# Optimization experiments

Measured on AMD Instinct MI355X. Metric: run time of the kernel, lower is better.

## Reference

```python
import jax, jax.numpy as jnp
import numpy as np

# Problem dimensions (match init_kwargs / input_specs)
B, NT = 4, 256          # shots, timesteps
NZ, NX = 384, 384       # domain
NREC = 128              # receivers
DT, DH = 0.001, 10.0    # time step [s], grid spacing [m]


def setup_inputs() -> dict:
    key = jax.random.key(0)
    k1, k2, k3, k4, k5, k6 = jax.random.split(key, 6)
    # source wavelets, one per shot: [B, NT]
    x = jax.random.normal(k1, (B, NT), dtype=jnp.float32)
    # velocity model 1500..3500 m/s: [NZ, NX]
    vp = 1500.0 + 2000.0 * jax.random.uniform(k2, (NZ, NX), dtype=jnp.float32)
    # per-shot source locations (kept away from the boundary)
    src_y = jax.random.randint(k3, (B,), 20, NZ - 20, dtype=jnp.int32)
    src_x = jax.random.randint(k4, (B,), 20, NX - 20, dtype=jnp.int32)
    # shared receiver array
    rec_y = jax.random.randint(k5, (NREC,), 20, NZ - 20, dtype=jnp.int32)
    rec_x = jax.random.randint(k6, (NREC,), 20, NX - 20, dtype=jnp.int32)
    return {"x": x, "vp": vp, "src_y": src_y, "src_x": src_x,
            "rec_y": rec_y, "rec_x": rec_x}


def _laplacian(u, inv_dh2):
    # 5-point stencil with zero (Dirichlet) boundaries; u: [B, NZ, NX]
    l = (u[:, 2:, 1:-1] + u[:, :-2, 1:-1]
         + u[:, 1:-1, 2:] + u[:, 1:-1, :-2]
         - 4.0 * u[:, 1:-1, 1:-1]) * inv_dh2
    return jnp.pad(l, ((0, 0), (1, 1), (1, 1)))


def reference(x, vp, src_y, src_x, rec_y, rec_x):
    """Second-order acoustic wave time-stepping with scatter source injection
    and receiver gather, as in WaveRNN.forward. Returns [NT, B, NREC] traces."""
    c2dt2 = (vp * DT) ** 2            # [NZ, NX], broadcast over shots
    inv_dh2 = jnp.float32(1.0 / (DH * DH))
    bidx = jnp.arange(B)

    def step(carry, xt):
        h1, h2 = carry                # current / previous wavefields [B,NZ,NX]
        hn = 2.0 * h1 - h2 + c2dt2 * _laplacian(h1, inv_dh2)
        hn = hn.at[bidx, src_y, src_x].add(xt)   # source injection (smask scatter)
        rec = hn[:, rec_y, rec_x]                 # receiver gather [B, NREC]
        return (hn, h1), rec

    h0 = jnp.zeros((B, NZ, NX), dtype=x.dtype)
    (_, _), y = jax.lax.scan(jax.checkpoint(step), (h0, h0), x.T)  # scan over time
    return y  # [NT, B, NREC]
```

## Files before the change

kernel.cpp:

```cpp
#include <hip/hip_runtime.h>

#define BB 4
#define NT 256
#define NZ 384
#define NX 384
#define NREC 128
#define NZX (NZ*NX)
#define BNZX (BB*NZX)
#define DT 0.001f
#define INV_DH2 0.01f

#define TILE 48
#define HALO 8
#define REGN 64
#define NBLK 256
#define NTHR 512
#define FSTRIDE 16

__global__ void wave_init(unsigned* flags) {
    int i = blockIdx.x * blockDim.x + threadIdx.x;
    if (i < NBLK * FSTRIDE) flags[i] = 0u;
}

__device__ inline float dpp_shl1(float v) {
    return __int_as_float(__builtin_amdgcn_update_dpp(
        0, __float_as_int(v), 0x130 , 0xf, 0xf, true));
}
__device__ inline float dpp_shr1(float v) {
    return __int_as_float(__builtin_amdgcn_update_dpp(
        0, __float_as_int(v), 0x138 , 0xf, 0xf, true));
}

__device__ inline void grid_sync(unsigned* flags, unsigned gen, int nbId) {
    __syncthreads();
    if (threadIdx.x < 64) {
        if (threadIdx.x == 0)
            __hip_atomic_store(&flags[blockIdx.x * FSTRIDE], gen,
                               __ATOMIC_RELAXED, __HIP_MEMORY_SCOPE_AGENT);
        for (;;) {
            unsigned f = __hip_atomic_load(&flags[nbId * FSTRIDE],
                             __ATOMIC_RELAXED, __HIP_MEMORY_SCOPE_AGENT);
            if (__all(f >= gen)) break;
            __builtin_amdgcn_s_sleep(1);
        }
    }
    __syncthreads();
}

__global__ __launch_bounds__(NTHR)
void wave_tiled(float* __restrict__ ws, const float* __restrict__ vp,
                const float* __restrict__ x,
                const int* __restrict__ src_y, const int* __restrict__ src_x,
                const int* __restrict__ rec_y, const int* __restrict__ rec_x,
                float* __restrict__ y) {
    __shared__ float bnd[2][16][REGN];
    __shared__ float recBuf[NREC][8];
    __shared__ float xs[NT];
    __shared__ int recLoc[NREC], recOut[NREC];
    __shared__ int recCnt;

    unsigned* flags = (unsigned*)(ws + 4*BNZX);

    const int tid = threadIdx.x;
    const int col = tid & 63;
    const int w   = tid >> 6;
    const int r0  = w << 3;
    const int blk = blockIdx.x;
    const int b  = blk >> 6;
    const int tz = (blk >> 3) & 7;
    const int tx = blk & 7;
    const int oz = tz*TILE - HALO, ox = tx*TILE - HALO;
    const int gx = ox + col;
    const int sy = src_y[b], sx = src_x[b];

    if (tid == 0) recCnt = 0;
    for (int k = tid; k < 16*REGN; k += NTHR) ((float*)bnd[0])[k] = 0.f;
    for (int k = tid; k < NT; k += NTHR) xs[k] = x[b*NT + k];
    __syncthreads();
    for (int r = tid; r < NREC; r += NTHR) {
        int ry = rec_y[r], rx = rec_x[r];
        if (ry/TILE == tz && rx/TILE == tx) {
            int p = atomicAdd(&recCnt, 1);
            recLoc[p] = ((ry - oz) << 6) | (rx - ox);
            recOut[p] = b*NREC + r;
        }
    }
    __syncthreads();

    int myN = 0, myM[4], myP[4];
    bool ovf = false;
    for (int p = 0; p < recCnt; ++p) {
        int rl = recLoc[p];
        if ((rl & 63) == col) {
            int rm = (rl >> 6) - r0;
            if ((unsigned)rm < 8u) {
                if (myN < 4) { myM[myN] = rm; myP[myN] = p; ++myN; }
                else ovf = true;
            }
        }
    }

    int nbId = blk;
    if (tid < 8) {
        int d = tid + (tid >= 4);
        int nz2 = tz + d/3 - 1, nx2 = tx + d%3 - 1;
        if ((unsigned)nz2 < 8u && (unsigned)nx2 < 8u)
            nbId = (b << 6) | (nz2 << 3) | nx2;
    }

    float cur[8], prv[8], c2i[8];
    #pragma unroll
    for (int m = 0; m < 8; ++m) {
        cur[m] = 0.f; prv[m] = 0.f;
        const int gz = oz + r0 + m;
        const bool inner = (gz > 0 && gz < NZ-1 && gx > 0 && gx < NX-1);
        const float v = inner ? vp[gz*NX + gx] * DT : 0.f;
        c2i[m] = v * v * INV_DH2;
    }
    const bool srcCol = (gx == sx);
    const int  srcM   = sy - oz - r0;
    const int  iuUp   = (2*w-1 < 0) ? 0 : 2*w-1;
    const int  iuDn   = (2*w+2 > 15) ? 15 : 2*w+2;
    __syncthreads();

    #pragma unroll 1
    for (int t = 0; t < NT; ++t) {
        const int pr = t & 1, pw = pr ^ 1;
        const float upB = bnd[pr][iuUp][col];
        const float dnB = bnd[pr][iuDn][col];

        float hn[8];
        #pragma unroll
        for (int m = 0; m < 8; ++m) {
            const float ce = cur[m];
            const float up = (m == 0) ? upB : cur[m-1];
            const float dn = (m == 7) ? dnB : cur[m+1];
            const float lf = dpp_shl1(ce);
            const float rt = dpp_shr1(ce);
            const float s  = (up + dn) + (lf + rt);
            hn[m] = fmaf(2.f, ce, -prv[m]) + c2i[m] * fmaf(-4.f, ce, s);
        }
        #pragma unroll
        for (int m = 0; m < 8; ++m) { prv[m] = cur[m]; cur[m] = hn[m]; }

        if (srcCol && (unsigned)srcM < 8u) {
            const float xv = xs[t];
            #pragma unroll
            for (int m = 0; m < 8; ++m) if (m == srcM) cur[m] += xv;
        }
        {
            const int s2 = t & 7;
            if (ovf) {
                for (int p = 0; p < recCnt; ++p) {
                    int rl = recLoc[p];
                    if ((rl & 63) == col) {
                        int rm = (rl >> 6) - r0;
                        if ((unsigned)rm < 8u) {
                            float v = cur[0];
                            #pragma unroll
                            for (int m = 1; m < 8; ++m) if (rm == m) v = cur[m];
                            recBuf[p][s2] = v;
                        }
                    }
                }
            } else {
                #pragma unroll
                for (int k = 0; k < 4; ++k) {
                    if (k < myN) {
                        float v = cur[0];
                        #pragma unroll
                        for (int m = 1; m < 8; ++m) if (myM[k] == m) v = cur[m];
                        recBuf[myP[k]][s2] = v;
                    }
                }
            }
        }
        bnd[pw][2*w  ][col] = cur[0];
        bnd[pw][2*w+1][col] = cur[7];

        if ((t & 7) == 7) {
            const int o = t >> 3;
            __syncthreads();
            for (int k = tid; k < recCnt*8; k += NTHR) {
                int p = k >> 3, s2 = k & 7;
                y[(size_t)((o<<3)+s2)*(BB*NREC) + recOut[p]] = recBuf[p][s2];
            }
            if (t < NT-1) {
                float* Gc = ws + (size_t)(o & 1) * 2*BNZX;
                float* Gp = Gc + BNZX;
                const bool colF = (col >= HALO   && col < REGN-HALO);
                const bool colM = (col >= 2*HALO && col < REGN-2*HALO);
                #pragma unroll
                for (int m = 0; m < 8; ++m) {
                    const int i = r0 + m;
                    const bool rowF = (i >= HALO   && i < REGN-HALO);
                    const bool rowM = (i >= 2*HALO && i < REGN-2*HALO);
                    if (colF && rowF && !(colM && rowM)) {
                        const size_t g = (size_t)b*NZX + (size_t)(oz+i)*NX + gx;
                        __hip_atomic_store(&Gc[g], cur[m],
                                           __ATOMIC_RELAXED, __HIP_MEMORY_SCOPE_AGENT);
                        __hip_atomic_store(&Gp[g], prv[m],
                                           __ATOMIC_RELAXED, __HIP_MEMORY_SCOPE_AGENT);
                    }
                }
                grid_sync(flags, (unsigned)(o + 1), nbId);
                const bool colH = (col < HALO || col >= REGN-HALO);
                const bool gxIn = (gx >= 0 && gx < NX);
                #pragma unroll
                for (int m = 0; m < 8; ++m) {
                    const int i = r0 + m;
                    if (colH || i < HALO || i >= REGN-HALO) {
                        const int gz = oz + i;
                        if (gxIn && gz >= 0 && gz < NZ) {
                            const size_t g = (size_t)b*NZX + (size_t)gz*NX + gx;
                            cur[m] = __hip_atomic_load(&Gc[g],
                                         __ATOMIC_RELAXED, __HIP_MEMORY_SCOPE_AGENT);
                            prv[m] = __hip_atomic_load(&Gp[g],
                                         __ATOMIC_RELAXED, __HIP_MEMORY_SCOPE_AGENT);
                        } else { cur[m] = 0.f; prv[m] = 0.f; }
                    }
                }
                bnd[pw][2*w  ][col] = cur[0];
                bnd[pw][2*w+1][col] = cur[7];
            }
        }
        __syncthreads();
    }
}

extern "C" void kernel_launch(void* const* d_in, const int* in_sizes, int n_in,
                              void* d_out, int out_size, void* d_ws, size_t ws_size,
                              hipStream_t stream) {
    const float* x     = (const float*)d_in[0];
    const float* vp    = (const float*)d_in[1];
    const int*   src_y = (const int*)d_in[2];
    const int*   src_x = (const int*)d_in[3];
    const int*   rec_y = (const int*)d_in[4];
    const int*   rec_x = (const int*)d_in[5];
    float* y  = (float*)d_out;
    float* ws = (float*)d_ws;

    wave_init<<<(NBLK*FSTRIDE + 255)/256, 256, 0, stream>>>((unsigned*)(ws + 4*BNZX));
    wave_tiled<<<NBLK, NTHR, 0, stream>>>(ws, vp, x, src_y, src_x, rec_y, rec_x, y);
}
```

Before: 275.4 us.

## Pack halo exchange into 64-bit stores and overlap receiver writes with grid sync

The separate cur/prv halo arrays are interleaved into one 64-bit word per cell, halving the number of atomic stores and loads during the periodic halo exchange. The receiver trace flush now runs on non-polling warps while the first wavefront spins on neighbor flags, and the s_sleep in the spin loop is removed. Halo loads use clamped addresses so all eight loads can be issued before they are consumed. In exchange, the tight spin loop without sleep may add memory traffic, and the layout needs a wider workspace stride.

```diff
diff --git a/kernel.cpp b/kernel.cpp
--- a/kernel.cpp
+++ b/kernel.cpp
@@ -31,20 +31,13 @@
         0, __float_as_int(v), 0x138 , 0xf, 0xf, true));
 }
 
-__device__ inline void grid_sync(unsigned* flags, unsigned gen, int nbId) {
-    __syncthreads();
-    if (threadIdx.x < 64) {
-        if (threadIdx.x == 0)
-            __hip_atomic_store(&flags[blockIdx.x * FSTRIDE], gen,
-                               __ATOMIC_RELAXED, __HIP_MEMORY_SCOPE_AGENT);
-        for (;;) {
-            unsigned f = __hip_atomic_load(&flags[nbId * FSTRIDE],
-                             __ATOMIC_RELAXED, __HIP_MEMORY_SCOPE_AGENT);
-            if (__all(f >= gen)) break;
-            __builtin_amdgcn_s_sleep(1);
-        }
-    }
-    __syncthreads();
+__device__ inline void stg2(unsigned long long* p, float a, float b) {
+    unsigned long long v = (unsigned long long)__float_as_uint(a)
+                         | ((unsigned long long)__float_as_uint(b) << 32);
+    __hip_atomic_store(p, v, __ATOMIC_RELAXED, __HIP_MEMORY_SCOPE_AGENT);
+}
+__device__ inline unsigned long long ldg2(const unsigned long long* p) {
+    return __hip_atomic_load(p, __ATOMIC_RELAXED, __HIP_MEMORY_SCOPE_AGENT);
 }
 
 __global__ __launch_bounds__(NTHR)
@@ -60,6 +53,8 @@
     __shared__ int recCnt;
 
     unsigned* flags = (unsigned*)(ws + 4*BNZX);
+    unsigned long long* F[2] = { (unsigned long long*)ws,
+                                 (unsigned long long*)ws + BNZX };
 
     const int tid = threadIdx.x;
     const int col = tid & 63;
@@ -121,6 +116,8 @@
     const int  srcM   = sy - oz - r0;
     const int  iuUp   = (2*w-1 < 0) ? 0 : 2*w-1;
     const int  iuDn   = (2*w+2 > 15) ? 15 : 2*w+2;
+    const bool gxIn = (gx >= 0 && gx < NX);
+    const int  gxc  = min(max(gx, 0), NX-1);
     __syncthreads();
 
     #pragma unroll 1
@@ -180,14 +177,8 @@
 
         if ((t & 7) == 7) {
             const int o = t >> 3;
-            __syncthreads();
-            for (int k = tid; k < recCnt*8; k += NTHR) {
-                int p = k >> 3, s2 = k & 7;
-                y[(size_t)((o<<3)+s2)*(BB*NREC) + recOut[p]] = recBuf[p][s2];
-            }
             if (t < NT-1) {
-                float* Gc = ws + (size_t)(o & 1) * 2*BNZX;
-                float* Gp = Gc + BNZX;
+                unsigned long long* Fw = F[o & 1];
                 const bool colF = (col >= HALO   && col < REGN-HALO);
                 const bool colM = (col >= 2*HALO && col < REGN-2*HALO);
                 #pragma unroll
@@ -195,33 +186,55 @@
                     const int i = r0 + m;
                     const bool rowF = (i >= HALO   && i < REGN-HALO);
                     const bool rowM = (i >= 2*HALO && i < REGN-2*HALO);
-                    if (colF && rowF && !(colM && rowM)) {
-                        const size_t g = (size_t)b*NZX + (size_t)(oz+i)*NX + gx;
-                        __hip_atomic_store(&Gc[g], cur[m],
+                    if (colF && rowF && !(colM && rowM))
+                        stg2(&Fw[(size_t)b*NZX + (size_t)(oz+i)*NX + gx],
+                             cur[m], prv[m]);
+                }
+                __syncthreads();
+                if (tid < 64) {
+                    if (tid == 0)
+                        __hip_atomic_store(&flags[blk * FSTRIDE], (unsigned)(o+1),
                                            __ATOMIC_RELAXED, __HIP_MEMORY_SCOPE_AGENT);
-                        __hip_atomic_store(&Gp[g], prv[m],
-                                           __ATOMIC_RELAXED, __HIP_MEMORY_SCOPE_AGENT);
-                    }
-                }
-                grid_sync(flags, (unsigned)(o + 1), nbId);
+                    for (;;) {
+                        unsigned f = __hip_atomic_load(&flags[nbId * FSTRIDE],
+                                         __ATOMIC_RELAXED, __HIP_MEMORY_SCOPE_AGENT);
+                        if (__all(f >= (unsigned)(o+1))) break;
+                    }
+                } else {
+                    for (int k = tid - 64; k < recCnt*8; k += NTHR - 64) {
+                        int p = k >> 3, s2 = k & 7;
+                        y[(size_t)((o<<3)+s2)*(BB*NREC) + recOut[p]] = recBuf[p][s2];
+                    }
+                }
+                __syncthreads();
                 const bool colH = (col < HALO || col >= REGN-HALO);
-                const bool gxIn = (gx >= 0 && gx < NX);
+                unsigned long long tmp[8];
+                bool ringm[8], valm[8];
                 #pragma unroll
                 for (int m = 0; m < 8; ++m) {
                     const int i = r0 + m;
-                    if (colH || i < HALO || i >= REGN-HALO) {
-                        const int gz = oz + i;
-                        if (gxIn && gz >= 0 && gz < NZ) {
-                            const size_t g = (size_t)b*NZX + (size_t)gz*NX + gx;
-                            cur[m] = __hip_atomic_load(&Gc[g],
-                                         __ATOMIC_RELAXED, __HIP_MEMORY_SCOPE_AGENT);
-                            prv[m] = __hip_atomic_load(&Gp[g],
-                                         __ATOMIC_RELAXED, __HIP_MEMORY_SCOPE_AGENT);
-                        } else { cur[m] = 0.f; prv[m] = 0.f; }
+                    const int gz = oz + i;
+                    ringm[m] = colH || i < HALO || i >= REGN-HALO;
+                    valm[m]  = gxIn && gz >= 0 && gz < NZ;
+                    const int gzc = min(max(gz, 0), NZ-1);
+                    if (ringm[m])
+                        tmp[m] = ldg2(&Fw[(size_t)b*NZX + (size_t)gzc*NX + gxc]);
+                }
+                #pragma unroll
+                for (int m = 0; m < 8; ++m) {
+                    if (ringm[m]) {
+                        cur[m] = valm[m] ? __uint_as_float((unsigned)tmp[m]) : 0.f;
+                        prv[m] = valm[m] ? __uint_as_float((unsigned)(tmp[m] >> 32)) : 0.f;
                     }
                 }
                 bnd[pw][2*w  ][col] = cur[0];
                 bnd[pw][2*w+1][col] = cur[7];
+            } else {
+                __syncthreads();
+                for (int k = tid; k < recCnt*8; k += NTHR) {
+                    int p = k >> 3, s2 = k & 7;
+                    y[(size_t)((o<<3)+s2)*(BB*NREC) + recOut[p]] = recBuf[p][s2];
+                }
             }
         }
         __syncthreads();
```

New measurement: 275.5 us. Within noise of the previous version (+0.0%).
